# Kernel tuning notes

Measured on AMD Instinct MI355X. Metric: run time of the kernel, lower is better.

## Reference

```python
import jax, jax.numpy as jnp
import numpy as np

N_NODES = 50000
N_EDGES = 800000
IN_DIM = 256
HID = 128


def setup_inputs() -> dict:
    key = jax.random.key(0)
    ks = jax.random.split(key, 8)
    x = jax.random.normal(ks[0], (N_NODES, IN_DIM), dtype=jnp.float32)
    edge_index = jax.random.randint(ks[1], (2, N_EDGES), 0, N_NODES, dtype=jnp.int32)
    edge_weight = jax.random.uniform(ks[2], (N_EDGES,), dtype=jnp.float32)
    # xavier_normal with gain=1.414 as in torch init
    g = 1.414
    W1 = jax.random.normal(ks[3], (HID, IN_DIM), dtype=jnp.float32) * (g * np.sqrt(2.0 / (HID + IN_DIM)))
    W2 = jax.random.normal(ks[4], (HID, HID), dtype=jnp.float32) * (g * np.sqrt(2.0 / (HID + HID)))
    b1 = jnp.zeros((HID,), dtype=jnp.float32)
    b2 = jnp.zeros((HID,), dtype=jnp.float32)
    a1 = jnp.full((1,), 0.25, dtype=jnp.float32)  # nn.PReLU() default init
    a2 = jnp.full((1,), 0.25, dtype=jnp.float32)
    return {"x": x, "edge_index": edge_index, "edge_weight": edge_weight,
            "W1": W1, "b1": b1, "a1": a1, "W2": W2, "b2": b2, "a2": a2}


def _gcn_layer(z, W, b, a, src, dst, w):
    # linear (no bias): [N, out]
    fts = z @ W.T
    # spmm: out[dst] += w * fts[src]
    msg = fts[src] * w[:, None]                      # [E, out]
    out = jax.ops.segment_sum(msg, dst, num_segments=N_NODES) + b
    # PReLU (single shared parameter)
    return jnp.where(out >= 0, out, a * out)


def reference(x, edge_index, edge_weight, W1, b1, a1, W2, b2, a2):
    src, dst = edge_index[0], edge_index[1]
    z = _gcn_layer(x, W1, b1, a1, src, dst, edge_weight)
    z = _gcn_layer(z, W2, b2, a2, src, dst, edge_weight)
    return z
```

## Files before the change

### kernel.cpp

```cpp
#include <hip/hip_runtime.h>

#define HID 128
#define BSH 6
#define BSZ 64
#define NBMAX 1024

typedef unsigned int uint;
typedef unsigned short ushort;
typedef __attribute__((ext_vector_type(8))) short short8;
typedef __attribute__((ext_vector_type(4))) float f32x4;

__device__ __forceinline__ uint pack_bf16x2(float a, float b) {
    uint ua = __float_as_uint(a);
    ua += 0x7fffu + ((ua >> 16) & 1u);
    uint ub = __float_as_uint(b);
    ub += 0x7fffu + ((ub >> 16) & 1u);
    return (ua >> 16) | (ub & 0xffff0000u);
}

__device__ __forceinline__ ushort bf16_of(float x) {
    uint u = __float_as_uint(x);
    u += 0x7fffu + ((u >> 16) & 1u);
    return (ushort)(u >> 16);
}

union FragAB { uint4 u; short8 s; };

__global__ __launch_bounds__(256) void w_to_frags_both(
    const float* __restrict__ W1, const float* __restrict__ W2,
    ushort* __restrict__ Wb1, ushort* __restrict__ Wb2, int* __restrict__ ghist) {
    int blk = blockIdx.x;
    if (blk == 24) {
        ((int4*)ghist)[threadIdx.x] = make_int4(0, 0, 0, 0);
        return;
    }
    const float* W = (blk < 16) ? W1 : W2;
    ushort* Wb = (blk < 16) ? Wb1 : Wb2;
    int K = (blk < 16) ? 256 : 128;
    int t = ((blk < 16) ? blk : blk - 16) * 256 + threadIdx.x;
    int lane = t & 63, f = t >> 6;
    int s = f >> 3, c = f & 7;
    int m = c * 16 + (lane & 15);
    int k0 = s * 32 + (lane >> 4) * 8;
    const float* wr = W + (size_t)m * K + k0;
    float4 a = *(const float4*)wr;
    float4 b = *(const float4*)(wr + 4);
    uint4 o = make_uint4(pack_bf16x2(a.x, a.y), pack_bf16x2(a.z, a.w),
                         pack_bf16x2(b.x, b.y), pack_bf16x2(b.z, b.w));
    *(uint4*)(Wb + (size_t)t * 8) = o;
}

template <int K, bool ABF16>
__global__ __launch_bounds__(256) void gemm_mfma(
    const void* __restrict__ Xv, const ushort* __restrict__ Wb,
    ushort* __restrict__ out, int N) {
    const int lane = threadIdx.x & 63;
    const int wid  = threadIdx.x >> 6;
    const int n0   = blockIdx.x * 64 + wid * 16;
    const int arow = n0 + (lane & 15);
    const bool okA = arow < N;
    const int kgrp = (lane >> 4) * 8;
    const float*  xrow_f = (const float*)Xv + (size_t)arow * K;
    const ushort* xrow_h = (const ushort*)Xv + (size_t)arow * K;

    f32x4 acc[8];
#pragma unroll
    for (int c = 0; c < 8; ++c) acc[c] = (f32x4){0.f, 0.f, 0.f, 0.f};

#pragma unroll
    for (int s = 0; s < K / 32; ++s) {
        const int k0 = s * 32 + kgrp;
        FragAB af;
        if (ABF16) {
            af.u = okA ? *(const uint4*)(xrow_h + k0) : make_uint4(0, 0, 0, 0);
        } else {
            float4 va = make_float4(0.f, 0.f, 0.f, 0.f), vb = va;
            if (okA) {
                va = *(const float4*)(xrow_f + k0);
                vb = *(const float4*)(xrow_f + k0 + 4);
            }
            af.u = make_uint4(pack_bf16x2(va.x, va.y), pack_bf16x2(va.z, va.w),
                              pack_bf16x2(vb.x, vb.y), pack_bf16x2(vb.z, vb.w));
        }
#pragma unroll
        for (int c = 0; c < 8; ++c) {
            FragAB bfr;
            bfr.u = *(const uint4*)(Wb + (size_t)((s * 8 + c) * 64 + lane) * 8);
            acc[c] = __builtin_amdgcn_mfma_f32_16x16x32_bf16(af.s, bfr.s, acc[c], 0, 0, 0);
        }
    }
    const int col = lane & 15;
    const int rbase = n0 + (lane >> 4) * 4;
#pragma unroll
    for (int c = 0; c < 8; ++c) {
#pragma unroll
        for (int r = 0; r < 4; ++r) {
            int n = rbase + r;
            if (n < N) out[(size_t)n * HID + c * 16 + col] = bf16_of(acc[c][r]);
        }
    }
}

__global__ __launch_bounds__(256) void bucket_hist(const int* __restrict__ dst,
                                                   int* __restrict__ ghist, int E, int NB) {
    __shared__ int h[NBMAX];
    for (int i = threadIdx.x; i < NB; i += 256) h[i] = 0;
    __syncthreads();
    int stride = gridDim.x * 256;
    for (int e = blockIdx.x * 256 + threadIdx.x; e < E; e += stride)
        atomicAdd(&h[dst[e] >> BSH], 1);
    __syncthreads();
    for (int i = threadIdx.x; i < NB; i += 256) {
        int c = h[i];
        if (c) atomicAdd(&ghist[i], c);
    }
}

__global__ __launch_bounds__(NBMAX) void bucket_scan(const int* __restrict__ ghist,
                                                     int* __restrict__ gbase,
                                                     int* __restrict__ gcur, int NB, int E) {
    __shared__ int l[NBMAX];
    int t = threadIdx.x;
    int v = (t < NB) ? ghist[t] : 0;
    l[t] = v;
    __syncthreads();
    int x = v;
    for (int o = 1; o < NBMAX; o <<= 1) {
        int y = (t >= o) ? l[t - o] : 0;
        __syncthreads();
        x += y;
        l[t] = x;
        __syncthreads();
    }
    if (t < NB) { gbase[t] = x - v; gcur[t] = x - v; }
    if (t == 0) gbase[NB] = E;
}

__global__ __launch_bounds__(256) void bucket_stage(
    const int* __restrict__ src, const int* __restrict__ dst,
    const float* __restrict__ w, int* __restrict__ gcur,
    int2* __restrict__ staged, int E, int NB) {
    __shared__ int lh[NBMAX], lb[NBMAX];
    for (int i = threadIdx.x; i < NB; i += 256) lh[i] = 0;
    __syncthreads();
    int chunk = (E + gridDim.x - 1) / gridDim.x;
    int c0 = blockIdx.x * chunk;
    int c1 = min(c0 + chunk, E);
    for (int e = c0 + threadIdx.x; e < c1; e += 256)
        atomicAdd(&lh[dst[e] >> BSH], 1);
    __syncthreads();
    for (int i = threadIdx.x; i < NB; i += 256) {
        int c = lh[i];
        lb[i] = c ? atomicAdd(&gcur[i], c) : 0;
        lh[i] = 0;
    }
    __syncthreads();
    for (int e = c0 + threadIdx.x; e < c1; e += 256) {
        int d = dst[e];
        int b = d >> BSH;
        int slot = lb[b] + atomicAdd(&lh[b], 1);
        staged[slot] = make_int2(src[e] | ((d & (BSZ - 1)) << 16), __float_as_int(w[e]));
    }
}

__global__ __launch_bounds__(256) void node_sort(
    const int* __restrict__ gbase, const int2* __restrict__ staged,
    int2* __restrict__ csr, int* __restrict__ off, int N) {
    __shared__ int hist[BSZ];
    __shared__ int cur[BSZ];
    const int b = blockIdx.x;
    const int s0 = gbase[b], s1 = gbase[b + 1];
    const int t = threadIdx.x;
    if (t < BSZ) hist[t] = 0;
    __syncthreads();
    for (int e = s0 + t; e < s1; e += 256)
        atomicAdd(&hist[(staged[e].x >> 16) & (BSZ - 1)], 1);
    __syncthreads();
    if (t < BSZ) {
        int x = hist[t];
        int incl = x;
#pragma unroll
        for (int o = 1; o < BSZ; o <<= 1) {
            int y = __shfl_up(incl, o, BSZ);
            if (t >= o) incl += y;
        }
        int excl = incl - x;
        cur[t] = excl;
        int n = (b << BSH) + t;
        if (n <= N) off[n] = s0 + excl;
    }
    __syncthreads();
    for (int e = s0 + t; e < s1; e += 256) {
        int2 m = staged[e];
        int d = (m.x >> 16) & (BSZ - 1);
        int p = atomicAdd(&cur[d], 1);
        csr[s0 + p] = m;
    }
}

template <bool OUTBF16>
__global__ __launch_bounds__(256) void csr_gather_bf16(
    const int* __restrict__ off, const int2* __restrict__ edges,
    const ushort* __restrict__ fts, void* __restrict__ outv,
    const float* __restrict__ bias, const float* __restrict__ alpha, int N) {
    int d = blockIdx.x * 4 + (threadIdx.x >> 6);
    if (d >= N) return;
    int lane = threadIdx.x & 63;
    int p = off[d], end = off[d + 1];
    float acc0 = 0.f, acc1 = 0.f;

#define ROWU(e) (*((const uint*)(fts + (size_t)((e).x & 0xffff) * HID) + lane))
#define LO(r) __uint_as_float((r) << 16)
#define HI(r) __uint_as_float((r) & 0xffff0000u)

    for (; p + 7 < end; p += 8) {
        int2 e[8];
        uint r[8];
#pragma unroll
        for (int i = 0; i < 8; ++i) e[i] = edges[p + i];
#pragma unroll
        for (int i = 0; i < 8; ++i) r[i] = ROWU(e[i]);
#pragma unroll
        for (int i = 0; i < 8; ++i) {
            float wt = __int_as_float(e[i].y);
            acc0 += wt * LO(r[i]);
            acc1 += wt * HI(r[i]);
        }
    }
    for (; p + 3 < end; p += 4) {
        int2 e0 = edges[p], e1 = edges[p + 1], e2 = edges[p + 2], e3 = edges[p + 3];
        uint r0 = ROWU(e0), r1 = ROWU(e1), r2 = ROWU(e2), r3 = ROWU(e3);
        float w0 = __int_as_float(e0.y), w1 = __int_as_float(e1.y);
        float w2 = __int_as_float(e2.y), w3 = __int_as_float(e3.y);
        acc0 += w0 * LO(r0) + w1 * LO(r1) + w2 * LO(r2) + w3 * LO(r3);
        acc1 += w0 * HI(r0) + w1 * HI(r1) + w2 * HI(r2) + w3 * HI(r3);
    }
    for (; p < end; ++p) {
        int2 e = edges[p];
        uint r = ROWU(e);
        float wt = __int_as_float(e.y);
        acc0 += wt * LO(r);
        acc1 += wt * HI(r);
    }
#undef ROWU
#undef LO
#undef HI

    float a = alpha[0];
    acc0 += bias[lane * 2 + 0];
    acc1 += bias[lane * 2 + 1];
    acc0 = acc0 >= 0.f ? acc0 : a * acc0;
    acc1 = acc1 >= 0.f ? acc1 : a * acc1;
    if (OUTBF16) {
        ((uint*)outv)[(size_t)d * (HID / 2) + lane] = pack_bf16x2(acc0, acc1);
    } else {
        *(float2*)&((float*)outv)[(size_t)d * HID + lane * 2] = make_float2(acc0, acc1);
    }
}

extern "C" void kernel_launch(void* const* d_in, const int* in_sizes, int n_in,
                              void* d_out, int out_size, void* d_ws, size_t ws_size,
                              hipStream_t stream) {
    const float* x  = (const float*)d_in[0];
    const int*   ei = (const int*)d_in[1];
    const float* ew = (const float*)d_in[2];
    const float* W1 = (const float*)d_in[3];
    const float* b1 = (const float*)d_in[4];
    const float* a1 = (const float*)d_in[5];
    const float* W2 = (const float*)d_in[6];
    const float* b2 = (const float*)d_in[7];
    const float* a2 = (const float*)d_in[8];
    float* out = (float*)d_out;

    int N = in_sizes[0] / 256;
    int E = in_sizes[2];
    const int* src = ei;
    const int* dst = ei + E;
    int NB = (N + BSZ - 1) >> BSH;

    ushort* fts    = (ushort*)d_ws;
    ushort* agg    = fts + (size_t)N * HID;
    int2*   staged = (int2*)(agg + (size_t)N * HID);
    int2*   csr    = staged + E;
    ushort* Wb1    = (ushort*)(csr + E);
    ushort* Wb2    = Wb1 + 128 * 256;
    int*    ghist  = (int*)(Wb2 + 128 * 128);
    int*    gbase  = ghist + NBMAX;
    int*    gcur   = gbase + NBMAX + 1;
    int*    off    = gcur + NBMAX;

    w_to_frags_both<<<25, 256, 0, stream>>>(W1, W2, Wb1, Wb2, ghist);

    bucket_hist<<<256, 256, 0, stream>>>(dst, ghist, E, NB);
    bucket_scan<<<1, NBMAX, 0, stream>>>(ghist, gbase, gcur, NB, E);
    bucket_stage<<<128, 256, 0, stream>>>(src, dst, ew, gcur, staged, E, NB);
    node_sort<<<NB, 256, 0, stream>>>(gbase, staged, csr, off, N);

    int gblk = (N + 63) / 64;
    int ggrid = (N + 3) / 4;

    gemm_mfma<256, false><<<gblk, 256, 0, stream>>>(x, Wb1, fts, N);
    csr_gather_bf16<true><<<ggrid, 256, 0, stream>>>(off, csr, fts, agg, b1, a1, N);

    gemm_mfma<128, true><<<gblk, 256, 0, stream>>>(agg, Wb2, fts, N);
    csr_gather_bf16<false><<<ggrid, 256, 0, stream>>>(off, csr, fts, out, b2, a2, N);
}
```

Before: 157.6 us.

## Double GEMM row tile per wave and split gather wave into four edge groups

The GEMM now computes 32 rows per wave with two accumulator sets, so each loaded W fragment feeds two MFMAs and the grid is halved. The CSR gather kernel is restructured so each wave splits into four 16-lane groups. Each lane loads 16 bytes (8 bf16 features) of a different edge's row, and the partial sums are reduced across groups with shuffles. This aims at wider vector gathers and more edges in flight per wave, at the cost of more accumulator registers and a cross-lane reduction.

```diff
diff --git a/kernel.cpp b/kernel.cpp
--- a/kernel.cpp
+++ b/kernel.cpp
@@ -51,52 +51,67 @@
 }
 
 template <int K, bool ABF16>
+__device__ __forceinline__ FragAB load_afrag(const void* __restrict__ Xv, int row,
+                                             int k0, bool ok) {
+    FragAB af;
+    if (ABF16) {
+        af.u = ok ? *(const uint4*)((const ushort*)Xv + (size_t)row * K + k0)
+                  : make_uint4(0, 0, 0, 0);
+    } else {
+        float4 va = make_float4(0.f, 0.f, 0.f, 0.f), vb = va;
+        if (ok) {
+            const float* xr = (const float*)Xv + (size_t)row * K + k0;
+            va = *(const float4*)xr;
+            vb = *(const float4*)(xr + 4);
+        }
+        af.u = make_uint4(pack_bf16x2(va.x, va.y), pack_bf16x2(va.z, va.w),
+                          pack_bf16x2(vb.x, vb.y), pack_bf16x2(vb.z, vb.w));
+    }
+    return af;
+}
+
+template <int K, bool ABF16>
 __global__ __launch_bounds__(256) void gemm_mfma(
     const void* __restrict__ Xv, const ushort* __restrict__ Wb,
     ushort* __restrict__ out, int N) {
     const int lane = threadIdx.x & 63;
     const int wid  = threadIdx.x >> 6;
-    const int n0   = blockIdx.x * 64 + wid * 16;
-    const int arow = n0 + (lane & 15);
-    const bool okA = arow < N;
+    const int n0   = blockIdx.x * 128 + wid * 32;
+    const int r0 = n0 + (lane & 15);
+    const int r1 = r0 + 16;
+    const bool ok0 = r0 < N, ok1 = r1 < N;
     const int kgrp = (lane >> 4) * 8;
-    const float*  xrow_f = (const float*)Xv + (size_t)arow * K;
-    const ushort* xrow_h = (const ushort*)Xv + (size_t)arow * K;
-
-    f32x4 acc[8];
-#pragma unroll
-    for (int c = 0; c < 8; ++c) acc[c] = (f32x4){0.f, 0.f, 0.f, 0.f};
+
+    f32x4 acc0[8], acc1[8];
+#pragma unroll
+    for (int c = 0; c < 8; ++c) {
+        acc0[c] = (f32x4){0.f, 0.f, 0.f, 0.f};
+        acc1[c] = (f32x4){0.f, 0.f, 0.f, 0.f};
+    }
 
 #pragma unroll
     for (int s = 0; s < K / 32; ++s) {
         const int k0 = s * 32 + kgrp;
-        FragAB af;
-        if (ABF16) {
-            af.u = okA ? *(const uint4*)(xrow_h + k0) : make_uint4(0, 0, 0, 0);
-        } else {
-            float4 va = make_float4(0.f, 0.f, 0.f, 0.f), vb = va;
-            if (okA) {
-                va = *(const float4*)(xrow_f + k0);
-                vb = *(const float4*)(xrow_f + k0 + 4);
-            }
-            af.u = make_uint4(pack_bf16x2(va.x, va.y), pack_bf16x2(va.z, va.w),
-                              pack_bf16x2(vb.x, vb.y), pack_bf16x2(vb.z, vb.w));
-        }
+        FragAB a0 = load_afrag<K, ABF16>(Xv, r0, k0, ok0);
+        FragAB a1 = load_afrag<K, ABF16>(Xv, r1, k0, ok1);
 #pragma unroll
         for (int c = 0; c < 8; ++c) {
             FragAB bfr;
             bfr.u = *(const uint4*)(Wb + (size_t)((s * 8 + c) * 64 + lane) * 8);
-            acc[c] = __builtin_amdgcn_mfma_f32_16x16x32_bf16(af.s, bfr.s, acc[c], 0, 0, 0);
+            acc0[c] = __builtin_amdgcn_mfma_f32_16x16x32_bf16(a0.s, bfr.s, acc0[c], 0, 0, 0);
+            acc1[c] = __builtin_amdgcn_mfma_f32_16x16x32_bf16(a1.s, bfr.s, acc1[c], 0, 0, 0);
         }
     }
     const int col = lane & 15;
-    const int rbase = n0 + (lane >> 4) * 4;
+    const int rb0 = n0 + (lane >> 4) * 4;
 #pragma unroll
     for (int c = 0; c < 8; ++c) {
 #pragma unroll
         for (int r = 0; r < 4; ++r) {
-            int n = rbase + r;
-            if (n < N) out[(size_t)n * HID + c * 16 + col] = bf16_of(acc[c][r]);
+            int na = rb0 + r;
+            if (na < N) out[(size_t)na * HID + c * 16 + col] = bf16_of(acc0[c][r]);
+            int nb = na + 16;
+            if (nb < N) out[(size_t)nb * HID + c * 16 + col] = bf16_of(acc1[c][r]);
         }
     }
 }
@@ -205,56 +220,67 @@
     const float* __restrict__ bias, const float* __restrict__ alpha, int N) {
     int d = blockIdx.x * 4 + (threadIdx.x >> 6);
     if (d >= N) return;
-    int lane = threadIdx.x & 63;
-    int p = off[d], end = off[d + 1];
-    float acc0 = 0.f, acc1 = 0.f;
-
-#define ROWU(e) (*((const uint*)(fts + (size_t)((e).x & 0xffff) * HID) + lane))
-#define LO(r) __uint_as_float((r) << 16)
-#define HI(r) __uint_as_float((r) & 0xffff0000u)
-
-    for (; p + 7 < end; p += 8) {
-        int2 e[8];
-        uint r[8];
-#pragma unroll
-        for (int i = 0; i < 8; ++i) e[i] = edges[p + i];
-#pragma unroll
-        for (int i = 0; i < 8; ++i) r[i] = ROWU(e[i]);
-#pragma unroll
-        for (int i = 0; i < 8; ++i) {
-            float wt = __int_as_float(e[i].y);
-            acc0 += wt * LO(r[i]);
-            acc1 += wt * HI(r[i]);
-        }
-    }
-    for (; p + 3 < end; p += 4) {
-        int2 e0 = edges[p], e1 = edges[p + 1], e2 = edges[p + 2], e3 = edges[p + 3];
-        uint r0 = ROWU(e0), r1 = ROWU(e1), r2 = ROWU(e2), r3 = ROWU(e3);
-        float w0 = __int_as_float(e0.y), w1 = __int_as_float(e1.y);
-        float w2 = __int_as_float(e2.y), w3 = __int_as_float(e3.y);
-        acc0 += w0 * LO(r0) + w1 * LO(r1) + w2 * LO(r2) + w3 * LO(r3);
-        acc1 += w0 * HI(r0) + w1 * HI(r1) + w2 * HI(r2) + w3 * HI(r3);
-    }
-    for (; p < end; ++p) {
-        int2 e = edges[p];
-        uint r = ROWU(e);
-        float wt = __int_as_float(e.y);
-        acc0 += wt * LO(r);
-        acc1 += wt * HI(r);
-    }
-#undef ROWU
-#undef LO
-#undef HI
-
-    float a = alpha[0];
-    acc0 += bias[lane * 2 + 0];
-    acc1 += bias[lane * 2 + 1];
-    acc0 = acc0 >= 0.f ? acc0 : a * acc0;
-    acc1 = acc1 >= 0.f ? acc1 : a * acc1;
-    if (OUTBF16) {
-        ((uint*)outv)[(size_t)d * (HID / 2) + lane] = pack_bf16x2(acc0, acc1);
-    } else {
-        *(float2*)&((float*)outv)[(size_t)d * HID + lane * 2] = make_float2(acc0, acc1);
+    const int lane = threadIdx.x & 63;
+    const int g = lane >> 4;
+    const int sub = lane & 15;
+    int p = off[d];
+    const int end = off[d + 1];
+    float acc[8];
+#pragma unroll
+    for (int j = 0; j < 8; ++j) acc[j] = 0.f;
+
+#define LOBITS(u_) __uint_as_float((u_) << 16)
+#define HIBITS(u_) __uint_as_float((u_) & 0xffff0000u)
+#define ACC8(R_, W_)                                              \
+    do {                                                          \
+        acc[0] += (W_) * LOBITS((R_).x); acc[1] += (W_) * HIBITS((R_).x); \
+        acc[2] += (W_) * LOBITS((R_).y); acc[3] += (W_) * HIBITS((R_).y); \
+        acc[4] += (W_) * LOBITS((R_).z); acc[5] += (W_) * HIBITS((R_).z); \
+        acc[6] += (W_) * LOBITS((R_).w); acc[7] += (W_) * HIBITS((R_).w); \
+    } while (0)
+
+    for (; p + 8 <= end; p += 8) {
+        int2 ma = edges[p + g];
+        int2 mb = edges[p + 4 + g];
+        uint4 ra = *(const uint4*)(fts + (size_t)(ma.x & 0xffff) * HID + sub * 8);
+        uint4 rb = *(const uint4*)(fts + (size_t)(mb.x & 0xffff) * HID + sub * 8);
+        float wa = __int_as_float(ma.y), wb = __int_as_float(mb.y);
+        ACC8(ra, wa);
+        ACC8(rb, wb);
+    }
+    for (; p < end; p += 4) {
+        int i = p + g;
+        int2 m = edges[(i < end) ? i : (end - 1)];
+        float wt = (i < end) ? __int_as_float(m.y) : 0.f;
+        uint4 r = *(const uint4*)(fts + (size_t)(m.x & 0xffff) * HID + sub * 8);
+        ACC8(r, wt);
+    }
+#undef ACC8
+#undef LOBITS
+#undef HIBITS
+
+#pragma unroll
+    for (int j = 0; j < 8; ++j) {
+        acc[j] += __shfl_xor(acc[j], 16);
+        acc[j] += __shfl_xor(acc[j], 32);
+    }
+
+    const float a = alpha[0];
+#pragma unroll
+    for (int j = 0; j < 8; ++j) {
+        float v = acc[j] + bias[sub * 8 + j];
+        acc[j] = v >= 0.f ? v : a * v;
+    }
+    if (g == 0) {
+        if (OUTBF16) {
+            uint4 o = make_uint4(pack_bf16x2(acc[0], acc[1]), pack_bf16x2(acc[2], acc[3]),
+                                 pack_bf16x2(acc[4], acc[5]), pack_bf16x2(acc[6], acc[7]));
+            *(uint4*)((ushort*)outv + (size_t)d * HID + sub * 8) = o;
+        } else {
+            float* op = (float*)outv + (size_t)d * HID + sub * 8;
+            *(float4*)op = make_float4(acc[0], acc[1], acc[2], acc[3]);
+            *(float4*)(op + 4) = make_float4(acc[4], acc[5], acc[6], acc[7]);
+        }
     }
 }
 
@@ -296,7 +322,7 @@
     bucket_stage<<<128, 256, 0, stream>>>(src, dst, ew, gcur, staged, E, NB);
     node_sort<<<NB, 256, 0, stream>>>(gbase, staged, csr, off, N);
 
-    int gblk = (N + 63) / 64;
+    int gblk = (N + 127) / 128;
     int ggrid = (N + 3) / 4;
 
     gemm_mfma<256, false><<<gblk, 256, 0, stream>>>(x, Wb1, fts, N);
```

Measured after the change: 153.0 us. 1.03x faster.
